# Optimization experiments

Measured on AMD Instinct MI355X. Metric: run time of the kernel, lower is better.

The kernel has to match this reference:

```python
import jax, jax.numpy as jnp
import numpy as np

MARGIN = 0.3
POS_THRESH_M = 25.0
NEG_THRESH_M = 100.0
EARTH_R = 6371000.0
B, D = 1024, 256


def _pairwise_haversine(gps):
    # gps: [B,2] degrees -> [B,B] meters
    lat = jnp.deg2rad(gps[:, 0])
    dlat = jnp.deg2rad(gps[None, :, 0] - gps[:, None, 0])
    dlon = jnp.deg2rad(gps[None, :, 1] - gps[:, None, 1])
    a = jnp.sin(dlat / 2) ** 2 + jnp.cos(lat)[:, None] * jnp.cos(lat)[None, :] * jnp.sin(dlon / 2) ** 2
    return EARTH_R * 2.0 * jnp.arctan2(jnp.sqrt(a), jnp.sqrt(1.0 - a))


def _pairwise_euclidean(emb):
    # faithful to torch.norm(emb[None]-emb[:,None], dim=-1), with safe sqrt at 0
    diff = emb[None, :, :] - emb[:, None, :]          # [B,B,D]
    sq = jnp.sum(diff * diff, axis=-1)                # [B,B]
    return jnp.where(sq > 0, jnp.sqrt(jnp.where(sq > 0, sq, 1.0)), 0.0)


def setup_inputs() -> dict:
    key = jax.random.key(0)
    k1, k2 = jax.random.split(key)
    embeddings = jax.random.normal(k1, (B, D), dtype=jnp.float32)
    # small geographic box (~222 m x ~182 m) so both positive (<25 m) and
    # negative (>100 m) pairs exist for nearly every anchor
    base = jnp.array([35.0, 139.0], dtype=jnp.float32)
    gps_coords = base + jax.random.uniform(k2, (B, 2), dtype=jnp.float32) * 0.002
    return {"embeddings": embeddings, "gps_coords": gps_coords}


def reference(embeddings, gps_coords):
    n = embeddings.shape[0]
    gps_d = _pairwise_haversine(gps_coords)           # [B,B]
    emb_d = _pairwise_euclidean(embeddings)           # [B,B]
    eye = jnp.eye(n, dtype=bool)
    pos_mask = (gps_d < POS_THRESH_M) & ~eye
    neg_mask = gps_d > NEG_THRESH_M

    has_pos = jnp.any(pos_mask, axis=1)
    has_neg = jnp.any(neg_mask, axis=1)
    valid = has_pos & has_neg                         # anchors contributing a triplet

    # hardest positive per anchor (masked max)
    d_ap = jnp.max(jnp.where(pos_mask, emb_d, -1.0), axis=1)          # [B]

    # semi-hard negatives: d_ap < d < d_ap + margin among negatives
    semi_mask = neg_mask & (emb_d > d_ap[:, None]) & (emb_d < d_ap[:, None] + MARGIN)
    has_semi = jnp.any(semi_mask, axis=1)
    BIG = jnp.float32(1e9)
    semi_min = jnp.min(jnp.where(semi_mask, emb_d, BIG), axis=1)
    neg_min = jnp.min(jnp.where(neg_mask, emb_d, BIG), axis=1)        # fallback: hardest negative
    d_an = jnp.where(has_semi, semi_min, neg_min)

    triplet = jax.nn.relu(d_ap - d_an + MARGIN)
    triplet = jnp.where(valid, triplet, 0.0)
    n_triplets = jnp.sum(valid.astype(jnp.float32))
    loss = jnp.sum(triplet) / jnp.maximum(n_triplets, 1.0)
    return loss
```

## Files before the change

kernel.cpp:

```cpp
#include <hip/hip_runtime.h>
#include <hip/hip_bf16.h>

typedef __attribute__((ext_vector_type(8))) short bf16x8;
typedef __attribute__((ext_vector_type(4))) float f32x4;

#define NB 1024
#define ND 256
#define MARGINF 0.3f
#define BIGV 1e9f
#define D2R 0.017453292519943295f
#define HD2R 0.008726646259971648f

#define A_POS 3.8495040e-12f
#define A_NEG 6.1592064e-11f

__device__ __forceinline__ float d4(float4 a, float4 b, float acc) {
    return fmaf(a.x,b.x, fmaf(a.y,b.y, fmaf(a.z,b.z, fmaf(a.w,b.w, acc))));
}

__device__ __forceinline__ void splitHL(float4 v0, float4 v1, bf16x8& H, bf16x8& L) {
    float f[8] = {v0.x, v0.y, v0.z, v0.w, v1.x, v1.y, v1.z, v1.w};
    #pragma unroll
    for (int q = 0; q < 8; ++q) {
        __hip_bfloat16 h = __float2bfloat16(f[q]);
        float hf = __bfloat162float(h);
        __hip_bfloat16 l = __float2bfloat16(f[q] - hf);
        H[q] = *(short*)&h;
        L[q] = *(short*)&l;
    }
}

__global__ __launch_bounds__(256) void gram_mfma(
    const float* __restrict__ emb, const float* __restrict__ gps,
    float* __restrict__ sEnc, float* __restrict__ pP)
{
    __shared__ float  sSqI[64], sSqJ[64];
    __shared__ float4 sGI[64], sGJ[64];
    __shared__ float  sRed[64][33];

    const int tid = threadIdx.x, lane = tid & 63, w = tid >> 6;
    const int wr = w >> 1, wc = w & 1;
    const int ib = blockIdx.x & 15, jb = blockIdx.x >> 4;
    const int i0 = ib*64, j0 = jb*64;
    const int lr = lane & 15, lk = lane >> 4;
    const float4* __restrict__ emb4 = (const float4*)emb;

    {
        const int half = tid & 1, r = (tid >> 1) & 63;
        const int base = (tid < 128) ? i0 : j0;
        const float4* rp = emb4 + (size_t)(base + r)*64 + half*32;
        float s = 0.f;
        #pragma unroll
        for (int q = 0; q < 32; ++q) s = d4(rp[q], rp[q], s);
        s += __shfl_xor(s, 1);
        if (half == 0) { if (tid < 128) sSqI[r] = s; else sSqJ[r] = s; }
    }
    if (tid < 128) {
        const int r = tid & 63;
        const int base = (tid < 64) ? i0 : j0;
        float2 g = ((const float2*)gps)[base + r];
        float4 gi = make_float4(g.x, g.y, cosf(g.x * D2R), 0.f);
        if (tid < 64) sGI[r] = gi; else sGJ[r] = gi;
    }
    __syncthreads();

    f32x4 acc[2][2] = {};
    #pragma unroll 2
    for (int k8 = 0; k8 < 8; ++k8) {
        const int co = k8*8 + lk*2;
        const float4* pa0 = emb4 + (size_t)(i0 + wr*32      + lr)*64 + co;
        const float4* pa1 = emb4 + (size_t)(i0 + wr*32 + 16 + lr)*64 + co;
        const float4* pb0 = emb4 + (size_t)(j0 + wc*32      + lr)*64 + co;
        const float4* pb1 = emb4 + (size_t)(j0 + wc*32 + 16 + lr)*64 + co;
        bf16x8 a0H,a0L,a1H,a1L,b0H,b0L,b1H,b1L;
        splitHL(pa0[0], pa0[1], a0H, a0L);
        splitHL(pa1[0], pa1[1], a1H, a1L);
        splitHL(pb0[0], pb0[1], b0H, b0L);
        splitHL(pb1[0], pb1[1], b1H, b1L);
        acc[0][0] = __builtin_amdgcn_mfma_f32_16x16x32_bf16(a0H, b0H, acc[0][0], 0,0,0);
        acc[0][1] = __builtin_amdgcn_mfma_f32_16x16x32_bf16(a0H, b1H, acc[0][1], 0,0,0);
        acc[1][0] = __builtin_amdgcn_mfma_f32_16x16x32_bf16(a1H, b0H, acc[1][0], 0,0,0);
        acc[1][1] = __builtin_amdgcn_mfma_f32_16x16x32_bf16(a1H, b1H, acc[1][1], 0,0,0);
        acc[0][0] = __builtin_amdgcn_mfma_f32_16x16x32_bf16(a0L, b0H, acc[0][0], 0,0,0);
        acc[0][1] = __builtin_amdgcn_mfma_f32_16x16x32_bf16(a0L, b1H, acc[0][1], 0,0,0);
        acc[1][0] = __builtin_amdgcn_mfma_f32_16x16x32_bf16(a1L, b0H, acc[1][0], 0,0,0);
        acc[1][1] = __builtin_amdgcn_mfma_f32_16x16x32_bf16(a1L, b1H, acc[1][1], 0,0,0);
        acc[0][0] = __builtin_amdgcn_mfma_f32_16x16x32_bf16(a0H, b0L, acc[0][0], 0,0,0);
        acc[0][1] = __builtin_amdgcn_mfma_f32_16x16x32_bf16(a0H, b1L, acc[0][1], 0,0,0);
        acc[1][0] = __builtin_amdgcn_mfma_f32_16x16x32_bf16(a1H, b0L, acc[1][0], 0,0,0);
        acc[1][1] = __builtin_amdgcn_mfma_f32_16x16x32_bf16(a1H, b1L, acc[1][1], 0,0,0);
    }

    float sqj[2]; float4 gj2[2];
    sqj[0] = sSqJ[wc*32 + lr];      gj2[0] = sGJ[wc*32 + lr];
    sqj[1] = sSqJ[wc*32 + 16 + lr]; gj2[1] = sGJ[wc*32 + 16 + lr];

    #pragma unroll
    for (int fi = 0; fi < 2; ++fi) {
        #pragma unroll
        for (int r = 0; r < 4; ++r) {
            const int rl = wr*32 + fi*16 + lk*4 + r;
            const int gi = i0 + rl;
            const float sqi = sSqI[rl];
            const float4 gvi = sGI[rl];
            float pmax = -1.f;
            #pragma unroll
            for (int fj = 0; fj < 2; ++fj) {
                const int gj = j0 + wc*32 + fj*16 + lr;
                float d2v = sqi + sqj[fj] - 2.f*acc[fi][fj][r];
                d2v = d2v > 0.f ? d2v : 0.f;
                const float sla = sinf((gj2[fj].x - gvi.x) * HD2R);
                const float slo = sinf((gj2[fj].y - gvi.y) * HD2R);
                const float hav = fmaf(sla, sla, (gvi.z * gj2[fj].z) * (slo*slo));
                const bool pos = (hav < A_POS) && (gi != gj);
                const bool neg = (hav > A_NEG);
                pmax = fmaxf(pmax, pos ? d2v : -1.f);
                sEnc[(size_t)gi*NB + gj] = neg ? d2v : BIGV;
            }
            sRed[rl][lr + 16*wc] = pmax;
        }
    }
    __syncthreads();
    if (tid < 64) {
        float m = sRed[tid][0];
        #pragma unroll
        for (int c = 1; c < 32; ++c) m = fmaxf(m, sRed[tid][c]);
        pP[(i0 + tid)*16 + jb] = m;
    }
}

__global__ __launch_bounds__(256) void rows_kernel(
    const float* __restrict__ sEnc, const float* __restrict__ pP,
    float* __restrict__ tri, float* __restrict__ val)
{
    const int tid = threadIdx.x, lane = tid & 63, w = tid >> 6;
    const int i = blockIdx.x*4 + w;

    float p = pP[i*16 + (lane & 15)];
    #pragma unroll
    for (int off = 1; off < 16; off <<= 1) p = fmaxf(p, __shfl_xor(p, off));
    const float dap2 = p;
    const bool has_pos = dap2 > -0.5f;
    float lo2 = -1.f, hi2 = -1.f;
    if (has_pos) { const float hb = sqrtf(dap2) + MARGINF; lo2 = dap2; hi2 = hb*hb; }

    float nmin = BIGV, smin = BIGV;
    const float4* __restrict__ row = (const float4*)sEnc + (size_t)i*256;
    #pragma unroll
    for (int pss = 0; pss < 4; ++pss) {
        const float4 x = row[pss*64 + lane];
        #pragma unroll
        for (int q = 0; q < 4; ++q) {
            const float xc = (q==0) ? x.x : (q==1) ? x.y : (q==2) ? x.z : x.w;
            nmin = fminf(nmin, xc);
            smin = fminf(smin, (xc > lo2 && xc < hi2) ? xc : BIGV);
        }
    }
    #pragma unroll
    for (int off = 1; off < 64; off <<= 1) {
        nmin = fminf(nmin, __shfl_xor(nmin, off));
        smin = fminf(smin, __shfl_xor(smin, off));
    }
    if (lane == 0) {
        const bool has_neg  = nmin < 0.5f*BIGV;
        const bool has_semi = smin < 0.5f*BIGV;
        const float dan2 = has_semi ? smin : nmin;
        const float dap  = has_pos ? sqrtf(dap2) : 0.f;
        float t = dap - sqrtf(dan2) + MARGINF;
        t = t > 0.f ? t : 0.f;
        const bool valid = has_pos && has_neg;
        tri[i] = valid ? t : 0.f;
        val[i] = valid ? 1.f : 0.f;
    }
}

__global__ __launch_bounds__(256) void finalize_kernel(
    const float* __restrict__ tri, const float* __restrict__ val, float* __restrict__ out)
{
    const int tid = threadIdx.x;
    float st = 0.f, sv = 0.f;
    #pragma unroll
    for (int g = 0; g < 4; ++g) { st += tri[tid + (g<<8)]; sv += val[tid + (g<<8)]; }
    #pragma unroll
    for (int off = 1; off < 64; off <<= 1) { st += __shfl_xor(st, off); sv += __shfl_xor(sv, off); }
    __shared__ float rt[4], rv[4];
    if ((tid & 63) == 0) { rt[tid>>6] = st; rv[tid>>6] = sv; }
    __syncthreads();
    if (tid == 0) {
        float t = rt[0]+rt[1]+rt[2]+rt[3];
        float v = rv[0]+rv[1]+rv[2]+rv[3];
        out[0] = t / fmaxf(v, 1.f);
    }
}

extern "C" void kernel_launch(void* const* d_in, const int* in_sizes, int n_in,
                              void* d_out, int out_size, void* d_ws, size_t ws_size,
                              hipStream_t stream) {
    const float* emb = (const float*)d_in[0];
    const float* gps = (const float*)d_in[1];
    float* ws = (float*)d_ws;

    float* sEnc = ws;
    float* pP   = ws + 1048576;
    float* tri  = pP + 16384;
    float* val  = tri + 1024;

    gram_mfma<<<256, 256, 0, stream>>>(emb, gps, sEnc, pP);
    rows_kernel<<<256, 256, 0, stream>>>(sEnc, pP, tri, val);
    finalize_kernel<<<1, 256, 0, stream>>>(tri, val, (float*)d_out);
}
```

Baseline: 27.42 us.

## Fuse finalize into row kernel via atomics and double gram block waves

The separate finalize launch is removed. Each rows block now atomically adds its triplet sum and valid count into workspace flags, and the last block to arrive, found through an atomic counter, writes the loss. The flags are zeroed by block 0 of the gram kernel. The gram kernel now uses 512 threads (8 waves) per 64x64 tile, with each wave owning a 32x16 sub-tile instead of 32x32, to raise occupancy and cut per-wave work. The atomic float adds make the summation order nondeterministic, and each wave reloads and splits its A operands, so the A-side load and split work is duplicated across more waves.

```diff
diff --git a/kernel.cpp b/kernel.cpp
--- a/kernel.cpp
+++ b/kernel.cpp
@@ -30,30 +30,33 @@
     }
 }
 
-__global__ __launch_bounds__(256) void gram_mfma(
+__global__ __launch_bounds__(512) void gram_mfma(
     const float* __restrict__ emb, const float* __restrict__ gps,
-    float* __restrict__ sEnc, float* __restrict__ pP)
+    float* __restrict__ sEnc, float* __restrict__ pP, float* __restrict__ flags)
 {
     __shared__ float  sSqI[64], sSqJ[64];
     __shared__ float4 sGI[64], sGJ[64];
-    __shared__ float  sRed[64][33];
+    __shared__ float  sRed[64][65];
 
     const int tid = threadIdx.x, lane = tid & 63, w = tid >> 6;
-    const int wr = w >> 1, wc = w & 1;
+    const int wr = w >> 2, wc = w & 3;
     const int ib = blockIdx.x & 15, jb = blockIdx.x >> 4;
     const int i0 = ib*64, j0 = jb*64;
     const int lr = lane & 15, lk = lane >> 4;
     const float4* __restrict__ emb4 = (const float4*)emb;
 
+    if (blockIdx.x == 0 && tid < 3) flags[tid] = 0.f;
+
     {
-        const int half = tid & 1, r = (tid >> 1) & 63;
-        const int base = (tid < 128) ? i0 : j0;
-        const float4* rp = emb4 + (size_t)(base + r)*64 + half*32;
+        const int q4 = tid & 3, r = (tid >> 2) & 63;
+        const int base = (tid < 256) ? i0 : j0;
+        const float4* rp = emb4 + (size_t)(base + r)*64 + q4*16;
         float s = 0.f;
         #pragma unroll
-        for (int q = 0; q < 32; ++q) s = d4(rp[q], rp[q], s);
+        for (int q = 0; q < 16; ++q) s = d4(rp[q], rp[q], s);
         s += __shfl_xor(s, 1);
-        if (half == 0) { if (tid < 128) sSqI[r] = s; else sSqJ[r] = s; }
+        s += __shfl_xor(s, 2);
+        if (q4 == 0) { if (tid < 256) sSqI[r] = s; else sSqJ[r] = s; }
     }
     if (tid < 128) {
         const int r = tid & 63;
@@ -64,75 +67,62 @@
     }
     __syncthreads();
 
-    f32x4 acc[2][2] = {};
+    f32x4 acc0 = {}, acc1 = {};
     #pragma unroll 2
     for (int k8 = 0; k8 < 8; ++k8) {
         const int co = k8*8 + lk*2;
         const float4* pa0 = emb4 + (size_t)(i0 + wr*32      + lr)*64 + co;
         const float4* pa1 = emb4 + (size_t)(i0 + wr*32 + 16 + lr)*64 + co;
-        const float4* pb0 = emb4 + (size_t)(j0 + wc*32      + lr)*64 + co;
-        const float4* pb1 = emb4 + (size_t)(j0 + wc*32 + 16 + lr)*64 + co;
-        bf16x8 a0H,a0L,a1H,a1L,b0H,b0L,b1H,b1L;
+        const float4* pb0 = emb4 + (size_t)(j0 + wc*16      + lr)*64 + co;
+        bf16x8 a0H,a0L,a1H,a1L,b0H,b0L;
         splitHL(pa0[0], pa0[1], a0H, a0L);
         splitHL(pa1[0], pa1[1], a1H, a1L);
         splitHL(pb0[0], pb0[1], b0H, b0L);
-        splitHL(pb1[0], pb1[1], b1H, b1L);
-        acc[0][0] = __builtin_amdgcn_mfma_f32_16x16x32_bf16(a0H, b0H, acc[0][0], 0,0,0);
-        acc[0][1] = __builtin_amdgcn_mfma_f32_16x16x32_bf16(a0H, b1H, acc[0][1], 0,0,0);
-        acc[1][0] = __builtin_amdgcn_mfma_f32_16x16x32_bf16(a1H, b0H, acc[1][0], 0,0,0);
-        acc[1][1] = __builtin_amdgcn_mfma_f32_16x16x32_bf16(a1H, b1H, acc[1][1], 0,0,0);
-        acc[0][0] = __builtin_amdgcn_mfma_f32_16x16x32_bf16(a0L, b0H, acc[0][0], 0,0,0);
-        acc[0][1] = __builtin_amdgcn_mfma_f32_16x16x32_bf16(a0L, b1H, acc[0][1], 0,0,0);
-        acc[1][0] = __builtin_amdgcn_mfma_f32_16x16x32_bf16(a1L, b0H, acc[1][0], 0,0,0);
-        acc[1][1] = __builtin_amdgcn_mfma_f32_16x16x32_bf16(a1L, b1H, acc[1][1], 0,0,0);
-        acc[0][0] = __builtin_amdgcn_mfma_f32_16x16x32_bf16(a0H, b0L, acc[0][0], 0,0,0);
-        acc[0][1] = __builtin_amdgcn_mfma_f32_16x16x32_bf16(a0H, b1L, acc[0][1], 0,0,0);
-        acc[1][0] = __builtin_amdgcn_mfma_f32_16x16x32_bf16(a1H, b0L, acc[1][0], 0,0,0);
-        acc[1][1] = __builtin_amdgcn_mfma_f32_16x16x32_bf16(a1H, b1L, acc[1][1], 0,0,0);
+        acc0 = __builtin_amdgcn_mfma_f32_16x16x32_bf16(a0H, b0H, acc0, 0,0,0);
+        acc1 = __builtin_amdgcn_mfma_f32_16x16x32_bf16(a1H, b0H, acc1, 0,0,0);
+        acc0 = __builtin_amdgcn_mfma_f32_16x16x32_bf16(a0L, b0H, acc0, 0,0,0);
+        acc1 = __builtin_amdgcn_mfma_f32_16x16x32_bf16(a1L, b0H, acc1, 0,0,0);
+        acc0 = __builtin_amdgcn_mfma_f32_16x16x32_bf16(a0H, b0L, acc0, 0,0,0);
+        acc1 = __builtin_amdgcn_mfma_f32_16x16x32_bf16(a1H, b0L, acc1, 0,0,0);
     }
 
-    float sqj[2]; float4 gj2[2];
-    sqj[0] = sSqJ[wc*32 + lr];      gj2[0] = sGJ[wc*32 + lr];
-    sqj[1] = sSqJ[wc*32 + 16 + lr]; gj2[1] = sGJ[wc*32 + 16 + lr];
+    const float  sqj = sSqJ[wc*16 + lr];
+    const float4 gj2 = sGJ[wc*16 + lr];
+    const int    gj  = j0 + wc*16 + lr;
 
     #pragma unroll
     for (int fi = 0; fi < 2; ++fi) {
+        const f32x4 a = fi ? acc1 : acc0;
         #pragma unroll
         for (int r = 0; r < 4; ++r) {
             const int rl = wr*32 + fi*16 + lk*4 + r;
             const int gi = i0 + rl;
-            const float sqi = sSqI[rl];
+            float d2v = sSqI[rl] + sqj - 2.f*a[r];
+            d2v = d2v > 0.f ? d2v : 0.f;
             const float4 gvi = sGI[rl];
-            float pmax = -1.f;
-            #pragma unroll
-            for (int fj = 0; fj < 2; ++fj) {
-                const int gj = j0 + wc*32 + fj*16 + lr;
-                float d2v = sqi + sqj[fj] - 2.f*acc[fi][fj][r];
-                d2v = d2v > 0.f ? d2v : 0.f;
-                const float sla = sinf((gj2[fj].x - gvi.x) * HD2R);
-                const float slo = sinf((gj2[fj].y - gvi.y) * HD2R);
-                const float hav = fmaf(sla, sla, (gvi.z * gj2[fj].z) * (slo*slo));
-                const bool pos = (hav < A_POS) && (gi != gj);
-                const bool neg = (hav > A_NEG);
-                pmax = fmaxf(pmax, pos ? d2v : -1.f);
-                sEnc[(size_t)gi*NB + gj] = neg ? d2v : BIGV;
-            }
-            sRed[rl][lr + 16*wc] = pmax;
+            const float sla = sinf((gj2.x - gvi.x) * HD2R);
+            const float slo = sinf((gj2.y - gvi.y) * HD2R);
+            const float hav = fmaf(sla, sla, (gvi.z * gj2.z) * (slo*slo));
+            const bool pos = (hav < A_POS) && (gi != gj);
+            const bool neg = (hav > A_NEG);
+            sEnc[(size_t)gi*NB + gj] = neg ? d2v : BIGV;
+            sRed[rl][wc*16 + lr] = pos ? d2v : -1.f;
         }
     }
     __syncthreads();
     if (tid < 64) {
         float m = sRed[tid][0];
         #pragma unroll
-        for (int c = 1; c < 32; ++c) m = fmaxf(m, sRed[tid][c]);
+        for (int c = 1; c < 64; ++c) m = fmaxf(m, sRed[tid][c]);
         pP[(i0 + tid)*16 + jb] = m;
     }
 }
 
-__global__ __launch_bounds__(256) void rows_kernel(
+__global__ __launch_bounds__(256) void rows_final(
     const float* __restrict__ sEnc, const float* __restrict__ pP,
-    float* __restrict__ tri, float* __restrict__ val)
+    float* __restrict__ flags, float* __restrict__ out)
 {
+    __shared__ float sT[4], sV[4];
     const int tid = threadIdx.x, lane = tid & 63, w = tid >> 6;
     const int i = blockIdx.x*4 + w;
 
@@ -169,27 +159,22 @@
         float t = dap - sqrtf(dan2) + MARGINF;
         t = t > 0.f ? t : 0.f;
         const bool valid = has_pos && has_neg;
-        tri[i] = valid ? t : 0.f;
-        val[i] = valid ? 1.f : 0.f;
+        sT[w] = valid ? t : 0.f;
+        sV[w] = valid ? 1.f : 0.f;
     }
-}
-
-__global__ __launch_bounds__(256) void finalize_kernel(
-    const float* __restrict__ tri, const float* __restrict__ val, float* __restrict__ out)
-{
-    const int tid = threadIdx.x;
-    float st = 0.f, sv = 0.f;
-    #pragma unroll
-    for (int g = 0; g < 4; ++g) { st += tri[tid + (g<<8)]; sv += val[tid + (g<<8)]; }
-    #pragma unroll
-    for (int off = 1; off < 64; off <<= 1) { st += __shfl_xor(st, off); sv += __shfl_xor(sv, off); }
-    __shared__ float rt[4], rv[4];
-    if ((tid & 63) == 0) { rt[tid>>6] = st; rv[tid>>6] = sv; }
     __syncthreads();
     if (tid == 0) {
-        float t = rt[0]+rt[1]+rt[2]+rt[3];
-        float v = rv[0]+rv[1]+rv[2]+rv[3];
-        out[0] = t / fmaxf(v, 1.f);
+        const float st = sT[0]+sT[1]+sT[2]+sT[3];
+        const float sv = sV[0]+sV[1]+sV[2]+sV[3];
+        atomicAdd(&flags[0], st);
+        atomicAdd(&flags[1], sv);
+        __threadfence();
+        const unsigned old = atomicAdd((unsigned*)&flags[2], 1u);
+        if (old == 255u) {
+            const float t = atomicAdd(&flags[0], 0.f);
+            const float v = atomicAdd(&flags[1], 0.f);
+            out[0] = t / fmaxf(v, 1.f);
+        }
     }
 }
 
@@ -200,12 +185,10 @@
     const float* gps = (const float*)d_in[1];
     float* ws = (float*)d_ws;
 
-    float* sEnc = ws;
-    float* pP   = ws + 1048576;
-    float* tri  = pP + 16384;
-    float* val  = tri + 1024;
+    float* sEnc  = ws;
+    float* pP    = ws + 1048576;
+    float* flags = pP + 16384;
 
-    gram_mfma<<<256, 256, 0, stream>>>(emb, gps, sEnc, pP);
-    rows_kernel<<<256, 256, 0, stream>>>(sEnc, pP, tri, val);
-    finalize_kernel<<<1, 256, 0, stream>>>(tri, val, (float*)d_out);
+    gram_mfma<<<256, 512, 0, stream>>>(emb, gps, sEnc, pP, flags);
+    rows_final<<<256, 256, 0, stream>>>(sEnc, pP, flags, (float*)d_out);
 }
```

New measurement: 37.68 us. +37.4%, slower.

## Fuse row reduction and finalize into gram kernel via last-block atomic counters

Applied to the files above, without the earlier changes.

Merges the three kernels into one. Each of the 16 column tiles of a row group bumps an atomic counter, and the last block to finish that group does the per-row semi-hard reductions. A second counter lets the final group-finisher write the loss. This removes two kernel launches and the inter-kernel gaps, but adds a memset, threadfences, and a serialized tail where only 16 blocks do the row work.

```diff
diff --git a/kernel.cpp b/kernel.cpp
--- a/kernel.cpp
+++ b/kernel.cpp
@@ -13,6 +13,11 @@
 
 #define A_POS 3.8495040e-12f
 #define A_NEG 6.1592064e-11f
+
+#define F_GSUM 0
+#define F_GCNT 1
+#define F_DONE 2
+#define F_GRP  3
 
 __device__ __forceinline__ float d4(float4 a, float4 b, float acc) {
     return fmaf(a.x,b.x, fmaf(a.y,b.y, fmaf(a.z,b.z, fmaf(a.w,b.w, acc))));
@@ -30,13 +35,16 @@
     }
 }
 
-__global__ __launch_bounds__(256) void gram_mfma(
+__global__ __launch_bounds__(256) void gram_fused(
     const float* __restrict__ emb, const float* __restrict__ gps,
-    float* __restrict__ sEnc, float* __restrict__ pP)
+    float* __restrict__ sEnc, float* __restrict__ pP,
+    float* __restrict__ flags, float* __restrict__ out)
 {
     __shared__ float  sSqI[64], sSqJ[64];
     __shared__ float4 sGI[64], sGJ[64];
     __shared__ float  sRed[64][33];
+    __shared__ float  sT[4], sV[4];
+    __shared__ int    sLast;
 
     const int tid = threadIdx.x, lane = tid & 63, w = tid >> 6;
     const int wr = w >> 1, wc = w & 1;
@@ -127,69 +135,72 @@
         for (int c = 1; c < 32; ++c) m = fmaxf(m, sRed[tid][c]);
         pP[(i0 + tid)*16 + jb] = m;
     }
-}
-
-__global__ __launch_bounds__(256) void rows_kernel(
-    const float* __restrict__ sEnc, const float* __restrict__ pP,
-    float* __restrict__ tri, float* __restrict__ val)
-{
-    const int tid = threadIdx.x, lane = tid & 63, w = tid >> 6;
-    const int i = blockIdx.x*4 + w;
-
-    float p = pP[i*16 + (lane & 15)];
-    #pragma unroll
-    for (int off = 1; off < 16; off <<= 1) p = fmaxf(p, __shfl_xor(p, off));
-    const float dap2 = p;
-    const bool has_pos = dap2 > -0.5f;
-    float lo2 = -1.f, hi2 = -1.f;
-    if (has_pos) { const float hb = sqrtf(dap2) + MARGINF; lo2 = dap2; hi2 = hb*hb; }
-
-    float nmin = BIGV, smin = BIGV;
-    const float4* __restrict__ row = (const float4*)sEnc + (size_t)i*256;
-    #pragma unroll
-    for (int pss = 0; pss < 4; ++pss) {
-        const float4 x = row[pss*64 + lane];
-        #pragma unroll
-        for (int q = 0; q < 4; ++q) {
-            const float xc = (q==0) ? x.x : (q==1) ? x.y : (q==2) ? x.z : x.w;
-            nmin = fminf(nmin, xc);
-            smin = fminf(smin, (xc > lo2 && xc < hi2) ? xc : BIGV);
-        }
-    }
-    #pragma unroll
-    for (int off = 1; off < 64; off <<= 1) {
-        nmin = fminf(nmin, __shfl_xor(nmin, off));
-        smin = fminf(smin, __shfl_xor(smin, off));
-    }
-    if (lane == 0) {
-        const bool has_neg  = nmin < 0.5f*BIGV;
-        const bool has_semi = smin < 0.5f*BIGV;
-        const float dan2 = has_semi ? smin : nmin;
-        const float dap  = has_pos ? sqrtf(dap2) : 0.f;
-        float t = dap - sqrtf(dan2) + MARGINF;
-        t = t > 0.f ? t : 0.f;
-        const bool valid = has_pos && has_neg;
-        tri[i] = valid ? t : 0.f;
-        val[i] = valid ? 1.f : 0.f;
-    }
-}
-
-__global__ __launch_bounds__(256) void finalize_kernel(
-    const float* __restrict__ tri, const float* __restrict__ val, float* __restrict__ out)
-{
-    const int tid = threadIdx.x;
-    float st = 0.f, sv = 0.f;
-    #pragma unroll
-    for (int g = 0; g < 4; ++g) { st += tri[tid + (g<<8)]; sv += val[tid + (g<<8)]; }
-    #pragma unroll
-    for (int off = 1; off < 64; off <<= 1) { st += __shfl_xor(st, off); sv += __shfl_xor(sv, off); }
-    __shared__ float rt[4], rv[4];
-    if ((tid & 63) == 0) { rt[tid>>6] = st; rv[tid>>6] = sv; }
+
+    __threadfence();
     __syncthreads();
     if (tid == 0) {
-        float t = rt[0]+rt[1]+rt[2]+rt[3];
-        float v = rv[0]+rv[1]+rv[2]+rv[3];
-        out[0] = t / fmaxf(v, 1.f);
+        const unsigned old = atomicAdd((unsigned*)&flags[F_GRP + ib], 1u);
+        sLast = (old == 15u) ? 1 : 0;
+    }
+    __syncthreads();
+    if (!sLast) return;
+
+    __threadfence();
+    float accT = 0.f, accV = 0.f;
+    #pragma unroll 2
+    for (int p = 0; p < 16; ++p) {
+        const int i = i0 + p*4 + w;
+        float pv = pP[i*16 + (lane & 15)];
+        #pragma unroll
+        for (int off = 1; off < 16; off <<= 1) pv = fmaxf(pv, __shfl_xor(pv, off));
+        const float dap2 = pv;
+        const bool has_pos = dap2 > -0.5f;
+        float lo2 = -1.f, hi2 = -1.f;
+        if (has_pos) { const float hb = sqrtf(dap2) + MARGINF; lo2 = dap2; hi2 = hb*hb; }
+
+        float nmin = BIGV, smin = BIGV;
+        const float4* __restrict__ row = (const float4*)sEnc + (size_t)i*256;
+        #pragma unroll
+        for (int pss = 0; pss < 4; ++pss) {
+            const float4 x = row[pss*64 + lane];
+            #pragma unroll
+            for (int q = 0; q < 4; ++q) {
+                const float xc = (q==0) ? x.x : (q==1) ? x.y : (q==2) ? x.z : x.w;
+                nmin = fminf(nmin, xc);
+                smin = fminf(smin, (xc > lo2 && xc < hi2) ? xc : BIGV);
+            }
+        }
+        #pragma unroll
+        for (int off = 1; off < 64; off <<= 1) {
+            nmin = fminf(nmin, __shfl_xor(nmin, off));
+            smin = fminf(smin, __shfl_xor(smin, off));
+        }
+        if (lane == 0) {
+            const bool has_neg  = nmin < 0.5f*BIGV;
+            const bool has_semi = smin < 0.5f*BIGV;
+            const float dan2 = has_semi ? smin : nmin;
+            const float dap  = has_pos ? sqrtf(dap2) : 0.f;
+            float t = dap - sqrtf(dan2) + MARGINF;
+            t = t > 0.f ? t : 0.f;
+            const bool valid = has_pos && has_neg;
+            accT += valid ? t : 0.f;
+            accV += valid ? 1.f : 0.f;
+        }
+    }
+    if (lane == 0) { sT[w] = accT; sV[w] = accV; }
+    __syncthreads();
+    if (tid == 0) {
+        const float st = sT[0]+sT[1]+sT[2]+sT[3];
+        const float sv = sV[0]+sV[1]+sV[2]+sV[3];
+        atomicAdd(&flags[F_GSUM], st);
+        atomicAdd(&flags[F_GCNT], sv);
+        __threadfence();
+        const unsigned old2 = atomicAdd((unsigned*)&flags[F_DONE], 1u);
+        if (old2 == 15u) {
+            const float t = atomicAdd(&flags[F_GSUM], 0.f);
+            const float v = atomicAdd(&flags[F_GCNT], 0.f);
+            out[0] = t / fmaxf(v, 1.f);
+        }
     }
 }
 
@@ -200,12 +211,10 @@
     const float* gps = (const float*)d_in[1];
     float* ws = (float*)d_ws;
 
-    float* sEnc = ws;
-    float* pP   = ws + 1048576;
-    float* tri  = pP + 16384;
-    float* val  = tri + 1024;
-
-    gram_mfma<<<256, 256, 0, stream>>>(emb, gps, sEnc, pP);
-    rows_kernel<<<256, 256, 0, stream>>>(sEnc, pP, tri, val);
-    finalize_kernel<<<1, 256, 0, stream>>>(tri, val, (float*)d_out);
-}
+    float* sEnc  = ws;
+    float* pP    = ws + 1048576;
+    float* flags = pP + 16384;
+
+    hipMemsetAsync(flags, 0, 19*sizeof(float), stream);
+    gram_fused<<<256, 256, 0, stream>>>(emb, gps, sEnc, pP, flags, (float*)d_out);
+}
```

Result: slower. 67.28 us (+145.4%).

## Split gram K-loop across two wave groups with shared-memory reduction

Applied to the files above, without the earlier changes.

Doubles the gram kernel block to 512 threads. Two groups of four waves each compute half of the K dimension, then combine their partial accumulators through LDS. The epilogue rows are then divided between the two groups. The aim is more waves per CU to hide global load latency on a grid of only 256 blocks. The cost is extra LDS traffic, two more barriers and a larger shared-memory footprint.

```diff
diff --git a/kernel.cpp b/kernel.cpp
--- a/kernel.cpp
+++ b/kernel.cpp
@@ -30,30 +30,33 @@
     }
 }
 
-__global__ __launch_bounds__(256) void gram_mfma(
+__global__ __launch_bounds__(512, 2) void gram_mfma(
     const float* __restrict__ emb, const float* __restrict__ gps,
     float* __restrict__ sEnc, float* __restrict__ pP)
 {
     __shared__ float  sSqI[64], sSqJ[64];
     __shared__ float4 sGI[64], sGJ[64];
     __shared__ float  sRed[64][33];
+    __shared__ float  sAcc[4*64*17];
 
     const int tid = threadIdx.x, lane = tid & 63, w = tid >> 6;
-    const int wr = w >> 1, wc = w & 1;
+    const int wq = w & 3, kh = w >> 2;
+    const int wr = wq >> 1, wc = wq & 1;
     const int ib = blockIdx.x & 15, jb = blockIdx.x >> 4;
     const int i0 = ib*64, j0 = jb*64;
     const int lr = lane & 15, lk = lane >> 4;
     const float4* __restrict__ emb4 = (const float4*)emb;
 
     {
-        const int half = tid & 1, r = (tid >> 1) & 63;
-        const int base = (tid < 128) ? i0 : j0;
-        const float4* rp = emb4 + (size_t)(base + r)*64 + half*32;
+        const int q4 = tid & 3, r = (tid >> 2) & 63;
+        const int base = (tid < 256) ? i0 : j0;
+        const float4* rp = emb4 + (size_t)(base + r)*64 + q4*16;
         float s = 0.f;
         #pragma unroll
-        for (int q = 0; q < 32; ++q) s = d4(rp[q], rp[q], s);
+        for (int q = 0; q < 16; ++q) s = d4(rp[q], rp[q], s);
         s += __shfl_xor(s, 1);
-        if (half == 0) { if (tid < 128) sSqI[r] = s; else sSqJ[r] = s; }
+        s += __shfl_xor(s, 2);
+        if (q4 == 0) { if (tid < 256) sSqI[r] = s; else sSqJ[r] = s; }
     }
     if (tid < 128) {
         const int r = tid & 63;
@@ -66,7 +69,8 @@
 
     f32x4 acc[2][2] = {};
     #pragma unroll 2
-    for (int k8 = 0; k8 < 8; ++k8) {
+    for (int kk8 = 0; kk8 < 4; ++kk8) {
+        const int k8 = kh*4 + kk8;
         const int co = k8*8 + lk*2;
         const float4* pa0 = emb4 + (size_t)(i0 + wr*32      + lr)*64 + co;
         const float4* pa1 = emb4 + (size_t)(i0 + wr*32 + 16 + lr)*64 + co;
@@ -91,34 +95,66 @@
         acc[1][1] = __builtin_amdgcn_mfma_f32_16x16x32_bf16(a1H, b1L, acc[1][1], 0,0,0);
     }
 
+    float* ab = &sAcc[(wq*64 + lane)*17];
+    if (kh == 1) {
+        #pragma unroll
+        for (int fi = 0; fi < 2; ++fi)
+            #pragma unroll
+            for (int fj = 0; fj < 2; ++fj)
+                #pragma unroll
+                for (int r = 0; r < 4; ++r)
+                    ab[fi*8 + fj*4 + r] = acc[fi][fj][r];
+    }
+    __syncthreads();
+    if (kh == 0) {
+        #pragma unroll
+        for (int fi = 0; fi < 2; ++fi)
+            #pragma unroll
+            for (int fj = 0; fj < 2; ++fj)
+                #pragma unroll
+                for (int r = 0; r < 4; ++r)
+                    acc[fi][fj][r] += ab[fi*8 + fj*4 + r];
+        #pragma unroll
+        for (int fj = 0; fj < 2; ++fj)
+            #pragma unroll
+            for (int r = 0; r < 4; ++r)
+                ab[8 + fj*4 + r] = acc[1][fj][r];
+    }
+    __syncthreads();
+    if (kh == 1) {
+        #pragma unroll
+        for (int fj = 0; fj < 2; ++fj)
+            #pragma unroll
+            for (int r = 0; r < 4; ++r)
+                acc[1][fj][r] = ab[8 + fj*4 + r];
+    }
+
     float sqj[2]; float4 gj2[2];
     sqj[0] = sSqJ[wc*32 + lr];      gj2[0] = sGJ[wc*32 + lr];
     sqj[1] = sSqJ[wc*32 + 16 + lr]; gj2[1] = sGJ[wc*32 + 16 + lr];
 
-    #pragma unroll
-    for (int fi = 0; fi < 2; ++fi) {
-        #pragma unroll
-        for (int r = 0; r < 4; ++r) {
-            const int rl = wr*32 + fi*16 + lk*4 + r;
-            const int gi = i0 + rl;
-            const float sqi = sSqI[rl];
-            const float4 gvi = sGI[rl];
-            float pmax = -1.f;
-            #pragma unroll
-            for (int fj = 0; fj < 2; ++fj) {
-                const int gj = j0 + wc*32 + fj*16 + lr;
-                float d2v = sqi + sqj[fj] - 2.f*acc[fi][fj][r];
-                d2v = d2v > 0.f ? d2v : 0.f;
-                const float sla = sinf((gj2[fj].x - gvi.x) * HD2R);
-                const float slo = sinf((gj2[fj].y - gvi.y) * HD2R);
-                const float hav = fmaf(sla, sla, (gvi.z * gj2[fj].z) * (slo*slo));
-                const bool pos = (hav < A_POS) && (gi != gj);
-                const bool neg = (hav > A_NEG);
-                pmax = fmaxf(pmax, pos ? d2v : -1.f);
-                sEnc[(size_t)gi*NB + gj] = neg ? d2v : BIGV;
-            }
-            sRed[rl][lr + 16*wc] = pmax;
+    const int fi = kh;
+    #pragma unroll
+    for (int r = 0; r < 4; ++r) {
+        const int rl = wr*32 + fi*16 + lk*4 + r;
+        const int gi = i0 + rl;
+        const float sqi = sSqI[rl];
+        const float4 gvi = sGI[rl];
+        float pmax = -1.f;
+        #pragma unroll
+        for (int fj = 0; fj < 2; ++fj) {
+            const int gj = j0 + wc*32 + fj*16 + lr;
+            float d2v = sqi + sqj[fj] - 2.f*acc[fi][fj][r];
+            d2v = d2v > 0.f ? d2v : 0.f;
+            const float sla = sinf((gj2[fj].x - gvi.x) * HD2R);
+            const float slo = sinf((gj2[fj].y - gvi.y) * HD2R);
+            const float hav = fmaf(sla, sla, (gvi.z * gj2[fj].z) * (slo*slo));
+            const bool pos = (hav < A_POS) && (gi != gj);
+            const bool neg = (hav > A_NEG);
+            pmax = fmaxf(pmax, pos ? d2v : -1.f);
+            sEnc[(size_t)gi*NB + gj] = neg ? d2v : BIGV;
         }
+        sRed[rl][lr + 16*wc] = pmax;
     }
     __syncthreads();
     if (tid < 64) {
@@ -205,7 +241,7 @@
     float* tri  = pP + 16384;
     float* val  = tri + 1024;
 
-    gram_mfma<<<256, 256, 0, stream>>>(emb, gps, sEnc, pP);
+    gram_mfma<<<256, 512, 0, stream>>>(emb, gps, sEnc, pP);
     rows_kernel<<<256, 256, 0, stream>>>(sEnc, pP, tri, val);
     finalize_kernel<<<1, 256, 0, stream>>>(tri, val, (float*)d_out);
 }
```

New measurement: 27.78 us. No clear change (+1.3%).
